# Performance work log

Hardware: AMD Instinct MI355X
Metric: run time of the kernel (lower is better)

Reference implementation:

```python
import jax, jax.numpy as jnp
import numpy as np

B, L, D, H = 2, 2048, 1024, 16
HD = D // H


def setup_inputs() -> dict:
    key = jax.random.key(0)
    ks = jax.random.split(key, 8)
    x = jax.random.normal(ks[0], (B, L, D), dtype=jnp.float32)
    WQ = jax.random.normal(ks[1], (D, D), dtype=jnp.float32) * 0.02
    bQ = jnp.zeros((D,), dtype=jnp.float32)
    WK = jax.random.normal(ks[2], (D, D), dtype=jnp.float32) * 0.02
    bK = jnp.zeros((D,), dtype=jnp.float32)
    WV = jax.random.normal(ks[3], (D, D), dtype=jnp.float32) * 0.02
    bV = jnp.zeros((D,), dtype=jnp.float32)
    Wc = jax.random.normal(ks[4], (D, D), dtype=jnp.float32) * 0.02  # dense channel-mix matrix [d_out, d_in]
    return {"x": x, "WQ": WQ, "bQ": bQ, "WK": WK, "bK": bK, "WV": WV, "bV": bV, "Wc": Wc}


def reference(x, WQ, bQ, WK, bK, WV, bV, Wc):
    b, l, d = x.shape
    # --- TokenMixWeightGenerator (LOW_RANK): T = softmax(causal(Q K^T / sqrt(hd)))
    q = (x @ WQ.T + bQ).reshape(b, l, H, HD).transpose(0, 2, 1, 3)  # [B,H,L,hd]
    k = (x @ WK.T + bK).reshape(b, l, H, HD).transpose(0, 2, 1, 3)  # [B,H,L,hd]
    scores = jnp.einsum("bhid,bhjd->bhij", q, k) / jnp.sqrt(jnp.float32(HD))
    causal_mask = jnp.tril(jnp.ones((l, l), dtype=bool))  # keep j <= i
    scores = jnp.where(causal_mask, scores, -jnp.inf)
    T = jax.nn.softmax(scores, axis=-1)  # [B,H,L,L] explicit token-mix matrix
    # --- UnifiedFeaturizer (expansion=1): V reshaped per head
    v = (x @ WV.T + bV).reshape(b, l, H, HD).transpose(0, 2, 1, 3)  # [B,H,L,hd]
    # --- Y = C @ (T @ V)
    mixed = jnp.einsum("bhij,bhjd->bhid", T, v)  # [B,H,L,hd]
    mixed = mixed.transpose(0, 2, 1, 3).reshape(b, l, d)  # [B,L,D]
    y = mixed @ Wc.T  # channel mixing: output = input @ W.T
    return y
```

## Files before the change

### kernel.cpp

```cpp
#include <hip/hip_runtime.h>


typedef __bf16 bf16x8 __attribute__((ext_vector_type(8)));
typedef float f32x4 __attribute__((ext_vector_type(4)));
typedef float f32x16 __attribute__((ext_vector_type(16)));
typedef unsigned short us4 __attribute__((ext_vector_type(4)));

#if defined(__has_builtin)
#if __has_builtin(__builtin_amdgcn_global_load_lds)
#define HAS_GLL 1
#endif
#if __has_builtin(__builtin_amdgcn_exp2f)
#define EXP2F(x) __builtin_amdgcn_exp2f(x)
#endif
#endif
#ifndef HAS_GLL
#define HAS_GLL 0
#endif
#ifndef EXP2F
#define EXP2F(x) exp2f(x)
#endif

__device__ __forceinline__ float bf2f(unsigned short u) {
    union { unsigned int i; float f; } v; v.i = ((unsigned int)u) << 16; return v.f;
}
__device__ __forceinline__ unsigned short f2bf(float f) {
    union { float f; unsigned int i; } v; v.f = f;
    unsigned int r = v.i + 0x7FFFu + ((v.i >> 16) & 1u);
    return (unsigned short)(r >> 16);
}
__device__ __forceinline__ f32x4 mfma16(bf16x8 a, bf16x8 b, f32x4 c) {
    return __builtin_amdgcn_mfma_f32_16x16x32_bf16(a, b, c, 0, 0, 0);
}
__device__ __forceinline__ f32x16 mfma32(bf16x8 a, bf16x8 b, f32x16 c) {
    return __builtin_amdgcn_mfma_f32_32x32x16_bf16(a, b, c, 0, 0, 0);
}
__device__ __forceinline__ float clamp4(float v) {
    return fminf(fmaxf(v, -1e4f), 1e4f);
}
union U8 { unsigned short s[8]; bf16x8 v; };

__device__ __forceinline__ unsigned int cvt_pk_bf16(float lo, float hi) {
    unsigned int r;
    asm("v_cvt_pk_bf16_f32 %0, %1, %2" : "=v"(r) : "v"(lo), "v"(hi));
    return r;
}
__device__ __forceinline__ void pl32swap(unsigned int& a, unsigned int& b) {
    asm volatile("v_permlane32_swap_b32 %0, %1" : "+v"(a), "+v"(b));
}

#if HAS_GLL
__device__ __forceinline__ void gl_lds16(const unsigned short* g, unsigned short* l) {
    __builtin_amdgcn_global_load_lds(
        (const __attribute__((address_space(1))) void*)g,
        (__attribute__((address_space(3))) void*)l, 16, 0, 0);
}
#endif


__global__ __launch_bounds__(256) void convert_all(
    const float* __restrict__ x, const float* __restrict__ WQ,
    const float* __restrict__ WK, const float* __restrict__ WV,
    const float* __restrict__ Wc,
    unsigned short* __restrict__ xbf, unsigned short* __restrict__ wbf)
{
    size_t e = ((size_t)blockIdx.x * 256 + threadIdx.x) * 8;
    const float* src; unsigned short* dst; size_t off;
    if (e < 4194304) { src = x; dst = xbf; off = e; }
    else {
        size_t j = e - 4194304; int sel = (int)(j >> 20); off = j & 1048575;
        src = (sel == 0) ? WQ : (sel == 1) ? WK : (sel == 2) ? WV : Wc;
        dst = wbf + (size_t)sel * 1048576;
    }
    f32x4 a = *(const f32x4*)(src + off);
    f32x4 b = *(const f32x4*)(src + off + 4);
    U8 u;
    u.s[0] = f2bf(a[0]); u.s[1] = f2bf(a[1]); u.s[2] = f2bf(a[2]); u.s[3] = f2bf(a[3]);
    u.s[4] = f2bf(b[0]); u.s[5] = f2bf(b[1]); u.s[6] = f2bf(b[2]); u.s[7] = f2bf(b[3]);
    *(bf16x8*)(dst + off) = u.v;
}

__global__ __launch_bounds__(256) void gemm128(
    const unsigned short* __restrict__ A, const unsigned short* __restrict__ Wbase,
    const float* __restrict__ b0, const float* __restrict__ b1, const float* __restrict__ b2,
    void* __restrict__ d0, void* __restrict__ d1, void* __restrict__ d2, int modeBase)
{
    const int z = blockIdx.z;
    const unsigned short* W = Wbase + (size_t)z * 1048576;
    const float* bias = (z == 0) ? b0 : (z == 1) ? b1 : b2;
    void* dst = (z == 0) ? d0 : (z == 1) ? d1 : d2;
    const int mode = modeBase + z;

    __shared__ __align__(16) unsigned short At[128][64];
    __shared__ __align__(16) unsigned short Bt[128][64];

    const int mb = blockIdx.y * 128, nb = blockIdx.x * 128;
    const int tid = threadIdx.x, w = tid >> 6, lane = tid & 63;
    const int wr = w >> 1, wc = w & 1;
    const int col = lane & 15, quad = lane >> 4;

    f32x4 acc[4][4];
    for (int i = 0; i < 4; ++i) for (int j = 0; j < 4; ++j) acc[i][j] = (f32x4){0.f, 0.f, 0.f, 0.f};

#if HAS_GLL
    const int srow8 = lane >> 3;
    const int scs   = (lane & 7) ^ srow8;
    const unsigned short* ga = A + (size_t)(mb + w * 32 + srow8) * 1024 + scs * 8;
    const unsigned short* gw = W + (size_t)(nb + w * 32 + srow8) * 1024 + scs * 8;
    unsigned short* lA0 = &At[w * 32][0];
    unsigned short* lA1 = &At[w * 32 + 8][0];
    unsigned short* lA2 = &At[w * 32 + 16][0];
    unsigned short* lA3 = &At[w * 32 + 24][0];
    unsigned short* lB0 = &Bt[w * 32][0];
    unsigned short* lB1 = &Bt[w * 32 + 8][0];
    unsigned short* lB2 = &Bt[w * 32 + 16][0];
    unsigned short* lB3 = &Bt[w * 32 + 24][0];
#else
    const int srow = tid >> 1;
    const int sc4  = (tid & 1) * 4;
    const unsigned short* Ab = A + (size_t)(mb + srow) * 1024;
    const unsigned short* Wb = W + (size_t)(nb + srow) * 1024;
#endif

    for (int kb = 0; kb < 1024; kb += 64) {
#if HAS_GLL
        gl_lds16(ga + kb, lA0);
        gl_lds16(ga + kb +  8 * 1024, lA1);
        gl_lds16(ga + kb + 16 * 1024, lA2);
        gl_lds16(ga + kb + 24 * 1024, lA3);
        gl_lds16(gw + kb, lB0);
        gl_lds16(gw + kb +  8 * 1024, lB1);
        gl_lds16(gw + kb + 16 * 1024, lB2);
        gl_lds16(gw + kb + 24 * 1024, lB3);
#else
        for (int cc = 0; cc < 4; ++cc) {
            const int ch = sc4 + cc, chs = ch ^ (srow & 7);
            *(bf16x8*)&At[srow][chs * 8] = *(const bf16x8*)(Ab + kb + ch * 8);
            *(bf16x8*)&Bt[srow][chs * 8] = *(const bf16x8*)(Wb + kb + ch * 8);
        }
#endif
        __syncthreads();
        bf16x8 a[4][2], b[4][2];
#pragma unroll
        for (int i = 0; i < 4; ++i) {
            const int ra = wr * 64 + i * 16 + col;
            const int rb = wc * 64 + i * 16 + col;
#pragma unroll
            for (int kk = 0; kk < 2; ++kk) {
                a[i][kk] = *(const bf16x8*)&At[ra][(((kk << 2) + quad) ^ (ra & 7)) << 3];
                b[i][kk] = *(const bf16x8*)&Bt[rb][(((kk << 2) + quad) ^ (rb & 7)) << 3];
            }
        }
#pragma unroll
        for (int kk = 0; kk < 2; ++kk)
#pragma unroll
            for (int i = 0; i < 4; ++i)
#pragma unroll
                for (int j = 0; j < 4; ++j)
                    acc[i][j] = mfma16(a[i][kk], b[j][kk], acc[i][j]);
        __syncthreads();
    }

    for (int i = 0; i < 4; ++i) {
        const int mbase = mb + wr * 64 + i * 16 + quad * 4;
        const int bb = mbase >> 11, l = mbase & 2047;
        for (int j = 0; j < 4; ++j) {
            const int n = nb + wc * 64 + j * 16 + col;
            const float bv = bias ? bias[n] : 0.f;
            if (mode == 3) {
                float* o = (float*)dst;
                for (int r = 0; r < 4; ++r)
                    o[(size_t)(mbase + r) * 1024 + n] = clamp4(acc[i][j][r] + bv);
            } else if (mode == 2) {
                const int h = n >> 6, hd = n & 63;
                us4 pk;
                for (int r = 0; r < 4; ++r) pk[r] = f2bf(clamp4(acc[i][j][r] + bv));
                *(us4*)((unsigned short*)dst + (size_t)(bb * 16 + h) * 131072
                        + (size_t)hd * 2048 + l) = pk;
            } else {
                const int h = n >> 6, hd = n & 63;
                unsigned short* o = (unsigned short*)dst + (size_t)(bb * 16 + h) * 131072
                                    + (size_t)l * 64 + hd;
                for (int r = 0; r < 4; ++r)
                    o[(size_t)r * 64] = f2bf(clamp4(acc[i][j][r] + bv));
            }
        }
    }
}


template<bool DIAG>
__device__ __forceinline__ void soft_pack(
    const f32x16& sacc, bf16x8* pa, float& lpart, int kg0, int qg)
{
    float p[16];
#pragma unroll
    for (int r = 0; r < 16; ++r) {
        float v = sacc[r] * 0.18033688f;
        if (DIAG) {
            int kg = kg0 + (r & 3) + 8 * (r >> 2);
            if (kg > qg) v = -1e30f;
        }
        v = fminf(v, 86.5f);
        p[r] = EXP2F(v);
    }
    float t0 = (p[0] + p[1]) + (p[2] + p[3]);
    float t1 = (p[4] + p[5]) + (p[6] + p[7]);
    float t2 = (p[8] + p[9]) + (p[10] + p[11]);
    float t3 = (p[12] + p[13]) + (p[14] + p[15]);
    lpart += (t0 + t1) + (t2 + t3);
#pragma unroll
    for (int c = 0; c < 2; ++c) {
        unsigned int a0 = cvt_pk_bf16(p[8*c + 0], p[8*c + 1]);
        unsigned int b0 = cvt_pk_bf16(p[8*c + 4], p[8*c + 5]);
        unsigned int a1 = cvt_pk_bf16(p[8*c + 2], p[8*c + 3]);
        unsigned int b1 = cvt_pk_bf16(p[8*c + 6], p[8*c + 7]);
        pl32swap(a0, b0);
        pl32swap(a1, b1);
        union PW { unsigned int w[4]; bf16x8 v; } pw;
        pw.w[0] = a0; pw.w[1] = a1; pw.w[2] = b0; pw.w[3] = b1;
        pa[c] = pw.v;
    }
}

template<bool DIAG>
__device__ __forceinline__ void attn32_step2(
    const unsigned short (*__restrict__ Kt)[72], const unsigned short* __restrict__ Vt,
    const bf16x8* __restrict__ qf, f32x16* __restrict__ oacc, float& lpart,
    int kb, int qg, int hi, int c31)
{
    f32x16 s0, s1;
#pragma unroll
    for (int r = 0; r < 16; ++r) { s0[r] = 0.f; s1[r] = 0.f; }
#pragma unroll
    for (int dc = 0; dc < 4; ++dc) {
        bf16x8 kf0 = *(const bf16x8*)&Kt[c31][dc * 16 + hi * 8];
        bf16x8 kf1 = *(const bf16x8*)&Kt[32 + c31][dc * 16 + hi * 8];
        s0 = mfma32(kf0, qf[dc], s0);
        s1 = mfma32(kf1, qf[dc], s1);
    }
    bf16x8 pa[4];
    soft_pack<DIAG>(s0, pa,     lpart, kb + 4 * hi,      qg);
    soft_pack<DIAG>(s1, pa + 2, lpart, kb + 32 + 4 * hi, qg);
#pragma unroll
    for (int b2 = 0; b2 < 2; ++b2)
#pragma unroll
        for (int kc = 0; kc < 4; ++kc) {
            bf16x8 vf = *(const bf16x8*)&Vt[(size_t)(b2 * 32 + c31) * 136 + kc * 16 + hi * 8];
            oacc[b2] = mfma32(pa[kc], vf, oacc[b2]);
        }
}

__device__ __forceinline__ void attn_write32(
    unsigned short* __restrict__ mixed, int gb, int h, int q0, int c31, int hi,
    const f32x16* __restrict__ oacc, const float* __restrict__ lrow)
{
    f32x4 iv[4];
#pragma unroll
    for (int m = 0; m < 4; ++m) {
        f32x4 lv = *(const f32x4*)&lrow[4 * hi + 8 * m];
#pragma unroll
        for (int r = 0; r < 4; ++r) iv[m][r] = 1.f / lv[r];
    }
#pragma unroll
    for (int b2 = 0; b2 < 2; ++b2)
#pragma unroll
        for (int r = 0; r < 16; ++r) {
            const int qrow = q0 + 4 * hi + (r & 3) + 8 * (r >> 2);
            const float val = clamp4(oacc[b2][r] * iv[r >> 2][r & 3]);
            mixed[(size_t)(gb * 2048 + qrow) * 1024 + h * 64 + b2 * 32 + c31] = f2bf(val);
        }
}

__global__ __launch_bounds__(256, 2) void attn32d(
    const unsigned short* __restrict__ Q, const unsigned short* __restrict__ K,
    const unsigned short* __restrict__ V, unsigned short* __restrict__ mixed)
{
    const int lb = blockIdx.x;
    const int i = lb & 255, kk = lb >> 8;
    const int bh = i & 31, j = i >> 5;
    const int A = kk ? (15 - j) : j;
    const int niter = A + 1;

    const int tid = threadIdx.x, w = tid >> 6, lane = tid & 63;
    const int c31 = lane & 31, hi = lane >> 5;

    __shared__ __align__(16) unsigned short Kt[128][72];
    __shared__ __align__(16) unsigned short Vt[64][136];
    __shared__ __align__(16) float lslab[4][32];

    const unsigned short* Qb = Q + (size_t)bh * 131072;
    const unsigned short* Kb = K + (size_t)bh * 131072;
    const unsigned short* Vb = V + (size_t)bh * 131072;

    const int q0 = A * 128 + w * 32;
    const int qg = q0 + c31;
    const int ss = 2 * A + (w >> 1);

    bf16x8 qf[4];
    {
        const unsigned short* Qr = Qb + (size_t)qg * 64 + hi * 8;
#pragma unroll
        for (int dc = 0; dc < 4; ++dc) qf[dc] = *(const bf16x8*)(Qr + dc * 16);
    }

    f32x16 oacc[2];
#pragma unroll
    for (int b2 = 0; b2 < 2; ++b2)
#pragma unroll
        for (int r = 0; r < 16; ++r) oacc[b2][r] = 0.f;
    float lpart = 0.f;

    const int sr = tid >> 3, sc = (tid & 7) * 8;

    const unsigned short* kp = Kb + (size_t)sr * 64 + sc;
    const unsigned short* vp = Vb + (size_t)sr * 2048 + sc;
    bf16x8 pk0 = *(const bf16x8*)kp;
    bf16x8 pk1 = *(const bf16x8*)(kp + 32 * 64);
    bf16x8 pk2 = *(const bf16x8*)(kp + 64 * 64);
    bf16x8 pk3 = *(const bf16x8*)(kp + 96 * 64);
    bf16x8 pv0 = *(const bf16x8*)vp;
    bf16x8 pv1 = *(const bf16x8*)(vp + 32 * 2048);
    bf16x8 pv2 = *(const bf16x8*)(vp + 64);
    bf16x8 pv3 = *(const bf16x8*)(vp + 32 * 2048 + 64);

    for (int jj = 0; jj < niter; ++jj) {
        __syncthreads();
        *(bf16x8*)&Kt[sr][sc]       = pk0;
        *(bf16x8*)&Kt[sr + 32][sc]  = pk1;
        *(bf16x8*)&Kt[sr + 64][sc]  = pk2;
        *(bf16x8*)&Kt[sr + 96][sc]  = pk3;
        *(bf16x8*)&Vt[sr][sc]       = pv0;
        *(bf16x8*)&Vt[sr + 32][sc]  = pv1;
        *(bf16x8*)&Vt[sr][64 + sc]  = pv2;
        *(bf16x8*)&Vt[sr + 32][64 + sc] = pv3;
        __syncthreads();
        if (jj + 1 < niter) {
            const int kb2 = (jj + 1) * 128;
            const unsigned short* kp2 = Kb + (size_t)(kb2 + sr) * 64 + sc;
            const unsigned short* vp2 = Vb + (size_t)sr * 2048 + kb2 + sc;
            pk0 = *(const bf16x8*)kp2;
            pk1 = *(const bf16x8*)(kp2 + 32 * 64);
            pk2 = *(const bf16x8*)(kp2 + 64 * 64);
            pk3 = *(const bf16x8*)(kp2 + 96 * 64);
            pv0 = *(const bf16x8*)vp2;
            pv1 = *(const bf16x8*)(vp2 + 32 * 2048);
            pv2 = *(const bf16x8*)(vp2 + 64);
            pv3 = *(const bf16x8*)(vp2 + 32 * 2048 + 64);
        }
        const int t0 = 2 * jj, t1 = t0 + 1;
        if (t0 < ss)
            attn32_step2<false>(&Kt[0], &Vt[0][0],  qf, oacc, lpart, t0 * 64, qg, hi, c31);
        else if (t0 == ss)
            attn32_step2<true >(&Kt[0], &Vt[0][0],  qf, oacc, lpart, t0 * 64, qg, hi, c31);
        if (t1 < ss)
            attn32_step2<false>(&Kt[64], &Vt[0][64], qf, oacc, lpart, t1 * 64, qg, hi, c31);
        else if (t1 == ss)
            attn32_step2<true >(&Kt[64], &Vt[0][64], qf, oacc, lpart, t1 * 64, qg, hi, c31);
    }

    float ltot = lpart + __shfl_xor(lpart, 32, 64);
    if (lane < 32) lslab[w][lane] = ltot;

    const int gb = bh >> 4, h = bh & 15;
    attn_write32(mixed, gb, h, q0, c31, hi, oacc, &lslab[w][0]);
}


__device__ __forceinline__ bf16x8 load8(const void* base, size_t eoff, int asF32) {
    if (asF32) {
        const float* p = (const float*)base + eoff;
        f32x4 a = *(const f32x4*)p;
        f32x4 b = *(const f32x4*)(p + 4);
        U8 u;
        u.s[0]=f2bf(a[0]); u.s[1]=f2bf(a[1]); u.s[2]=f2bf(a[2]); u.s[3]=f2bf(a[3]);
        u.s[4]=f2bf(b[0]); u.s[5]=f2bf(b[1]); u.s[6]=f2bf(b[2]); u.s[7]=f2bf(b[3]);
        return u.v;
    }
    return *(const bf16x8*)((const unsigned short*)base + eoff);
}

__global__ void dtype_probe(const unsigned short* __restrict__ x, int* __restrict__ flag) {
    if (threadIdx.x == 0) {
        int c = 0;
        for (int i = 0; i < 128; ++i) {
            int e = (x[2 * i] >> 7) & 0xFF;
            if (e >= 100 && e <= 135) ++c;
        }
        *flag = (c < 64) ? 1 : 0;
    }
}

__global__ __launch_bounds__(256) void gemm_bt(
    const void* __restrict__ Ap, const void* __restrict__ Wp,
    const void* __restrict__ biasp, void* __restrict__ dout,
    unsigned short* __restrict__ wsdst, const int* __restrict__ flag,
    long aOff, long outOff, int mode, int aFlagged)
{
    const int f32 = *flag;
    __shared__ __align__(16) unsigned short At[64][32];
    __shared__ __align__(16) unsigned short Bt[64][32];
    const int mb = blockIdx.y * 64, nb = blockIdx.x * 64;
    const int tid = threadIdx.x;
    const int w = tid >> 6, lane = tid & 63;
    const int wr = w >> 1, wc = w & 1;
    const int col = lane & 15, quad = lane >> 4;
    const int srow = tid >> 2, schunk = (tid & 3) * 8;
    const int aF = aFlagged && f32;

    f32x4 acc[2][2];
    for (int i = 0; i < 2; ++i) for (int j = 0; j < 2; ++j) acc[i][j] = (f32x4){0.f,0.f,0.f,0.f};

    const size_t aBase = (size_t)aOff + (size_t)(mb + srow) * 1024 + schunk;
    const size_t wBase = (size_t)(nb + srow) * 1024 + schunk;

    for (int kb = 0; kb < 1024; kb += 32) {
        *(bf16x8*)(&At[srow][schunk]) = load8(Ap, aBase + kb, aF);
        *(bf16x8*)(&Bt[srow][schunk]) = load8(Wp, wBase + kb, f32);
        __syncthreads();
        bf16x8 a0 = *(const bf16x8*)(&At[wr * 32 + col][quad * 8]);
        bf16x8 a1 = *(const bf16x8*)(&At[wr * 32 + 16 + col][quad * 8]);
        bf16x8 b0 = *(const bf16x8*)(&Bt[wc * 32 + col][quad * 8]);
        bf16x8 b1 = *(const bf16x8*)(&Bt[wc * 32 + 16 + col][quad * 8]);
        acc[0][0] = mfma16(a0, b0, acc[0][0]);
        acc[0][1] = mfma16(a0, b1, acc[0][1]);
        acc[1][0] = mfma16(a1, b0, acc[1][0]);
        acc[1][1] = mfma16(a1, b1, acc[1][1]);
        __syncthreads();
    }

    for (int mi = 0; mi < 2; ++mi) {
        for (int ni = 0; ni < 2; ++ni) {
            int n = nb + wc * 32 + ni * 16 + col;
            float bv = 0.f;
            if (biasp) bv = f32 ? ((const float*)biasp)[n] : bf2f(((const unsigned short*)biasp)[n]);
            for (int r = 0; r < 4; ++r) {
                int m = mb + wr * 32 + mi * 16 + quad * 4 + r;
                float v = clamp4(acc[mi][ni][r] + bv);
                if (mode == 3) {
                    size_t idx = (size_t)outOff + (size_t)m * 1024 + n;
                    if (f32) ((float*)dout)[idx] = v;
                    else     ((unsigned short*)dout)[idx] = f2bf(v);
                } else {
                    int h = n >> 6, hd = n & 63;
                    size_t idx = (mode == 2)
                        ? (size_t)h * 131072 + (size_t)hd * 2048 + m
                        : (size_t)h * 131072 + (size_t)m * 64 + hd;
                    unsigned short* dstp = (mode == 0)
                        ? (unsigned short*)dout + (f32 ? 4194304 : 2097152)
                        : wsdst;
                    dstp[idx] = f2bf(v);
                }
            }
        }
    }
}

__global__ __launch_bounds__(256) void attn_kernel(
    const void* __restrict__ dout, const unsigned short* __restrict__ Kw,
    const unsigned short* __restrict__ Vw, unsigned short* __restrict__ mixed,
    const int* __restrict__ flag)
{
    const int f32 = *flag;
    const int qtile = blockIdx.x;
    const int h = blockIdx.y;
    const int w = threadIdx.x >> 6, lane = threadIdx.x & 63;
    const int col = lane & 15, quad = lane >> 4;

    __shared__ __align__(16) unsigned short Plds[4][16][64];

    const unsigned short* Qs = (const unsigned short*)dout + (f32 ? 4194304 : 2097152);
    const unsigned short* Qb = Qs + (size_t)h * 131072;
    const unsigned short* Kb = Kw + (size_t)h * 131072;
    const unsigned short* Vb = Vw + (size_t)h * 131072;

    const int q0 = qtile * 64 + w * 16;
    bf16x8 aq0 = *(const bf16x8*)(Qb + (size_t)(q0 + col) * 64 + quad * 8);
    bf16x8 aq1 = *(const bf16x8*)(Qb + (size_t)(q0 + col) * 64 + 32 + quad * 8);

    float m_run[4] = {-1e30f, -1e30f, -1e30f, -1e30f};
    float l_run[4] = {0.f, 0.f, 0.f, 0.f};
    f32x4 oacc[4];
    for (int i = 0; i < 4; ++i) oacc[i] = (f32x4){0.f, 0.f, 0.f, 0.f};

    for (int kt = 0; kt <= qtile; ++kt) {
        const int kb = kt * 64;
        f32x4 s[4];
        for (int t = 0; t < 4; ++t) {
            s[t] = (f32x4){0.f, 0.f, 0.f, 0.f};
            bf16x8 bk0 = *(const bf16x8*)(Kb + (size_t)(kb + t * 16 + col) * 64 + quad * 8);
            bf16x8 bk1 = *(const bf16x8*)(Kb + (size_t)(kb + t * 16 + col) * 64 + 32 + quad * 8);
            s[t] = mfma16(aq0, bk0, s[t]);
            s[t] = mfma16(aq1, bk1, s[t]);
        }
        for (int t = 0; t < 4; ++t)
            for (int r = 0; r < 4; ++r) {
                float v = clamp4(s[t][r] * 0.125f);
                if (kt == qtile && (t * 16 + col > w * 16 + quad * 4 + r)) v = -1e30f;
                s[t][r] = v;
            }
        float mt[4];
        for (int r = 0; r < 4; ++r)
            mt[r] = fmaxf(fmaxf(s[0][r], s[1][r]), fmaxf(s[2][r], s[3][r]));
        for (int off = 1; off < 16; off <<= 1)
            for (int r = 0; r < 4; ++r)
                mt[r] = fmaxf(mt[r], __shfl_xor(mt[r], off, 64));
        float alpha[4], rs[4], p[4][4];
        for (int r = 0; r < 4; ++r) {
            float mn = fmaxf(m_run[r], mt[r]);
            alpha[r] = __expf(m_run[r] - mn);
            m_run[r] = mn;
        }
        for (int t = 0; t < 4; ++t)
            for (int r = 0; r < 4; ++r)
                p[t][r] = __expf(s[t][r] - m_run[r]);
        for (int r = 0; r < 4; ++r)
            rs[r] = (p[0][r] + p[1][r]) + (p[2][r] + p[3][r]);
        for (int off = 1; off < 16; off <<= 1)
            for (int r = 0; r < 4; ++r)
                rs[r] += __shfl_xor(rs[r], off, 64);
        for (int r = 0; r < 4; ++r)
            l_run[r] = l_run[r] * alpha[r] + rs[r];
        for (int nt = 0; nt < 4; ++nt)
            for (int r = 0; r < 4; ++r)
                oacc[nt][r] *= alpha[r];
        for (int t = 0; t < 4; ++t)
            for (int r = 0; r < 4; ++r)
                Plds[w][quad * 4 + r][t * 16 + col] = f2bf(p[t][r]);
        __syncthreads();
        bf16x8 ap0 = *(const bf16x8*)(&Plds[w][col][quad * 8]);
        bf16x8 ap1 = *(const bf16x8*)(&Plds[w][col][32 + quad * 8]);
        for (int nt = 0; nt < 4; ++nt) {
            bf16x8 bv0 = *(const bf16x8*)(Vb + (size_t)(nt * 16 + col) * 2048 + kb + quad * 8);
            bf16x8 bv1 = *(const bf16x8*)(Vb + (size_t)(nt * 16 + col) * 2048 + kb + 32 + quad * 8);
            oacc[nt] = mfma16(ap0, bv0, oacc[nt]);
            oacc[nt] = mfma16(ap1, bv1, oacc[nt]);
        }
        __syncthreads();
    }

    float inv[4];
    for (int r = 0; r < 4; ++r) inv[r] = 1.f / l_run[r];
    for (int nt = 0; nt < 4; ++nt)
        for (int r = 0; r < 4; ++r) {
            int qrow = q0 + quad * 4 + r;
            mixed[(size_t)qrow * 1024 + h * 64 + nt * 16 + col] = f2bf(clamp4(oacc[nt][r] * inv[r]));
        }
}


extern "C" void kernel_launch(void* const* d_in, const int* in_sizes, int n_in,
                              void* d_out, int out_size, void* d_ws, size_t ws_size,
                              hipStream_t stream) {
    (void)in_sizes; (void)n_in; (void)out_size;
    const void* x  = d_in[0];
    const void* WQ = d_in[1]; const void* bQ = d_in[2];
    const void* WK = d_in[3]; const void* bK = d_in[4];
    const void* WV = d_in[5]; const void* bV = d_in[6];
    const void* Wc = d_in[7];

    if (ws_size >= (size_t)32 * 1024 * 1024) {
        unsigned short* wbf   = (unsigned short*)d_ws;
        unsigned short* Kst   = wbf + 4194304;
        unsigned short* VTst  = Kst + 4194304;
        unsigned short* mixed = VTst + 4194304;
        unsigned short* xbf   = (unsigned short*)d_out;
        unsigned short* Qst   = xbf + 4194304;

        convert_all<<<4096, 256, 0, stream>>>(
            (const float*)x, (const float*)WQ, (const float*)WK,
            (const float*)WV, (const float*)Wc, xbf, wbf);

        gemm128<<<dim3(8, 32, 3), 256, 0, stream>>>(
            xbf, wbf, (const float*)bQ, (const float*)bK, (const float*)bV,
            Qst, Kst, VTst, 0);

        attn32d<<<dim3(512, 1), 256, 0, stream>>>(Qst, Kst, VTst, mixed);

        gemm128<<<dim3(8, 32, 1), 256, 0, stream>>>(
            mixed, wbf + 3145728, nullptr, nullptr, nullptr,
            d_out, nullptr, nullptr, 3);
    } else {
        unsigned short* wsK = (unsigned short*)d_ws;
        unsigned short* wsV = wsK + 2097152;
        unsigned short* wsM = wsV + 2097152;
        int* flag = (int*)((char*)d_ws + 12 * 1024 * 1024);

        dtype_probe<<<1, 64, 0, stream>>>((const unsigned short*)x, flag);

        dim3 gg(16, 32), gb(256);
        for (int b = 0; b < 2; ++b) {
            long xo = (long)b * 2048 * 1024;
            gemm_bt<<<gg, gb, 0, stream>>>(x, WQ, bQ, d_out, nullptr, flag, xo, 0, 0, 1);
            gemm_bt<<<gg, gb, 0, stream>>>(x, WK, bK, d_out, wsK, flag, xo, 0, 1, 1);
            gemm_bt<<<gg, gb, 0, stream>>>(x, WV, bV, d_out, wsV, flag, xo, 0, 2, 1);
            attn_kernel<<<dim3(32, 16), 256, 0, stream>>>(d_out, wsK, wsV, wsM, flag);
            gemm_bt<<<gg, gb, 0, stream>>>(wsM, Wc, nullptr, d_out, nullptr, flag,
                                           0, (long)b * 2048 * 1024, 3, 0);
        }
    }
}
```

Measured before the change: 179.4 us.

## Fuse Q/K/V projections into one GEMM kernel sharing the A tile

Replaces the three-slice gemm128 launch (grid z=3) with a dedicated gemmqkv kernel that loads each x tile once and multiplies it against the WQ, WK and WV tiles in the same K loop. The aim is to cut repeated A-tile global loads and LDS staging, at the cost of three times the accumulator registers (192 floats per lane), a larger LDS footprint and a third as many workgroups (256 blocks), with launch bounds forcing one block per SIMD set. The risks are lower occupancy and fewer blocks to fill the GPU.

```diff
diff --git a/kernel.cpp b/kernel.cpp
--- a/kernel.cpp
+++ b/kernel.cpp
@@ -78,6 +78,136 @@
     u.s[0] = f2bf(a[0]); u.s[1] = f2bf(a[1]); u.s[2] = f2bf(a[2]); u.s[3] = f2bf(a[3]);
     u.s[4] = f2bf(b[0]); u.s[5] = f2bf(b[1]); u.s[6] = f2bf(b[2]); u.s[7] = f2bf(b[3]);
     *(bf16x8*)(dst + off) = u.v;
+}
+
+__global__ __launch_bounds__(256, 1) void gemmqkv(
+    const unsigned short* __restrict__ A, const unsigned short* __restrict__ Wbase,
+    const float* __restrict__ b0, const float* __restrict__ b1, const float* __restrict__ b2,
+    void* __restrict__ d0, void* __restrict__ d1, void* __restrict__ d2)
+{
+    __shared__ __align__(16) unsigned short At[128][64];
+    __shared__ __align__(16) unsigned short Bt[3][128][64];
+
+    const int mb = blockIdx.y * 128, nb = blockIdx.x * 128;
+    const int tid = threadIdx.x, w = tid >> 6, lane = tid & 63;
+    const int wr = w >> 1, wc = w & 1;
+    const int col = lane & 15, quad = lane >> 4;
+
+    f32x4 acc[3][4][4];
+#pragma unroll
+    for (int zz = 0; zz < 3; ++zz)
+#pragma unroll
+        for (int i = 0; i < 4; ++i)
+#pragma unroll
+            for (int j = 0; j < 4; ++j)
+                acc[zz][i][j] = (f32x4){0.f, 0.f, 0.f, 0.f};
+
+#if HAS_GLL
+    const int srow8 = lane >> 3;
+    const int scs   = (lane & 7) ^ srow8;
+    const unsigned short* ga = A + (size_t)(mb + w * 32 + srow8) * 1024 + scs * 8;
+    const unsigned short* gw = Wbase + (size_t)(nb + w * 32 + srow8) * 1024 + scs * 8;
+
+    for (int kb = 0; kb < 1024; kb += 64) {
+#pragma unroll
+        for (int c = 0; c < 4; ++c)
+            gl_lds16(ga + kb + c * 8 * 1024, &At[w * 32 + 8 * c][0]);
+#pragma unroll
+        for (int zz = 0; zz < 3; ++zz)
+#pragma unroll
+            for (int c = 0; c < 4; ++c)
+                gl_lds16(gw + (size_t)zz * 1048576 + kb + c * 8 * 1024,
+                         &Bt[zz][w * 32 + 8 * c][0]);
+        __syncthreads();
+        bf16x8 a[4][2];
+#pragma unroll
+        for (int i = 0; i < 4; ++i) {
+            const int ra = wr * 64 + i * 16 + col;
+#pragma unroll
+            for (int kk = 0; kk < 2; ++kk)
+                a[i][kk] = *(const bf16x8*)&At[ra][(((kk << 2) + quad) ^ (ra & 7)) << 3];
+        }
+#pragma unroll
+        for (int zz = 0; zz < 3; ++zz) {
+            bf16x8 b[4][2];
+#pragma unroll
+            for (int j = 0; j < 4; ++j) {
+                const int rb = wc * 64 + j * 16 + col;
+#pragma unroll
+                for (int kk = 0; kk < 2; ++kk)
+                    b[j][kk] = *(const bf16x8*)&Bt[zz][rb][(((kk << 2) + quad) ^ (rb & 7)) << 3];
+            }
+#pragma unroll
+            for (int kk = 0; kk < 2; ++kk)
+#pragma unroll
+                for (int i = 0; i < 4; ++i)
+#pragma unroll
+                    for (int j = 0; j < 4; ++j)
+                        acc[zz][i][j] = mfma16(a[i][kk], b[j][kk], acc[zz][i][j]);
+        }
+        __syncthreads();
+    }
+#else
+    const int srow = tid >> 1;
+    const int sc4  = (tid & 1) * 4;
+    const unsigned short* Ab = A + (size_t)(mb + srow) * 1024;
+    for (int kb = 0; kb < 1024; kb += 64) {
+        for (int cc = 0; cc < 4; ++cc) {
+            const int ch = sc4 + cc, chs = ch ^ (srow & 7);
+            *(bf16x8*)&At[srow][chs * 8] = *(const bf16x8*)(Ab + kb + ch * 8);
+            for (int zz = 0; zz < 3; ++zz) {
+                const unsigned short* Wb = Wbase + (size_t)zz * 1048576 + (size_t)(nb + srow) * 1024;
+                *(bf16x8*)&Bt[zz][srow][chs * 8] = *(const bf16x8*)(Wb + kb + ch * 8);
+            }
+        }
+        __syncthreads();
+        bf16x8 a[4][2];
+        for (int i = 0; i < 4; ++i) {
+            const int ra = wr * 64 + i * 16 + col;
+            for (int kk = 0; kk < 2; ++kk)
+                a[i][kk] = *(const bf16x8*)&At[ra][(((kk << 2) + quad) ^ (ra & 7)) << 3];
+        }
+        for (int zz = 0; zz < 3; ++zz) {
+            bf16x8 b[4][2];
+            for (int j = 0; j < 4; ++j) {
+                const int rb = wc * 64 + j * 16 + col;
+                for (int kk = 0; kk < 2; ++kk)
+                    b[j][kk] = *(const bf16x8*)&Bt[zz][rb][(((kk << 2) + quad) ^ (rb & 7)) << 3];
+            }
+            for (int kk = 0; kk < 2; ++kk)
+                for (int i = 0; i < 4; ++i)
+                    for (int j = 0; j < 4; ++j)
+                        acc[zz][i][j] = mfma16(a[i][kk], b[j][kk], acc[zz][i][j]);
+        }
+        __syncthreads();
+    }
+#endif
+
+#pragma unroll
+    for (int zz = 0; zz < 3; ++zz) {
+        const float* bias = (zz == 0) ? b0 : (zz == 1) ? b1 : b2;
+        void* dst = (zz == 0) ? d0 : (zz == 1) ? d1 : d2;
+        for (int i = 0; i < 4; ++i) {
+            const int mbase = mb + wr * 64 + i * 16 + quad * 4;
+            const int bb = mbase >> 11, l = mbase & 2047;
+            for (int j = 0; j < 4; ++j) {
+                const int n = nb + wc * 64 + j * 16 + col;
+                const float bv = bias ? bias[n] : 0.f;
+                const int h = n >> 6, hd = n & 63;
+                if (zz == 2) {
+                    us4 pk;
+                    for (int r = 0; r < 4; ++r) pk[r] = f2bf(clamp4(acc[zz][i][j][r] + bv));
+                    *(us4*)((unsigned short*)dst + (size_t)(bb * 16 + h) * 131072
+                            + (size_t)hd * 2048 + l) = pk;
+                } else {
+                    unsigned short* o = (unsigned short*)dst + (size_t)(bb * 16 + h) * 131072
+                                        + (size_t)l * 64 + hd;
+                    for (int r = 0; r < 4; ++r)
+                        o[(size_t)r * 64] = f2bf(clamp4(acc[zz][i][j][r] + bv));
+                }
+            }
+        }
+    }
 }
 
 __global__ __launch_bounds__(256) void gemm128(
@@ -571,9 +701,9 @@
             (const float*)x, (const float*)WQ, (const float*)WK,
             (const float*)WV, (const float*)Wc, xbf, wbf);
 
-        gemm128<<<dim3(8, 32, 3), 256, 0, stream>>>(
+        gemmqkv<<<dim3(8, 32), 256, 0, stream>>>(
             xbf, wbf, (const float*)bQ, (const float*)bK, (const float*)bV,
-            Qst, Kst, VTst, 0);
+            Qst, Kst, VTst);
 
         attn32d<<<dim3(512, 1), 256, 0, stream>>>(Qst, Kst, VTst, mixed);
 
```

Result: slower. 200.2 us (+11.6%).
